# Performance work log

Hardware: AMD Instinct MI355X
Metric: run time of the kernel (lower is better)

## Reference

```python
import jax, jax.numpy as jnp
import numpy as np

B, H, W, C = 32, 56, 56, 256
K = 7  # spatial-attention conv kernel size


def setup_inputs() -> dict:
    key = jax.random.key(0)
    kx, kw = jax.random.split(key)
    x = jax.random.normal(kx, (B, H, W, C), dtype=jnp.float32)
    # he_normal init for a 7x7 conv with 2 input channels
    fan_in = K * K * 2
    conv_w = jax.random.normal(kw, (K, K, 2, 1), dtype=jnp.float32) * jnp.sqrt(2.0 / fan_in)
    return {"x": x, "conv_w": conv_w}


def reference(x, conv_w):
    # channel-wise avg and max pooling -> [B,H,W,2]
    avg_pool = jnp.mean(x, axis=-1, keepdims=True)
    max_pool = jnp.max(x, axis=-1, keepdims=True)
    concat = jnp.concatenate([avg_pool, max_pool], axis=-1)
    # 7x7 conv, 2 -> 1 channels, SAME padding, no bias, sigmoid activation
    attn = jax.lax.conv_general_dilated(
        concat, conv_w,
        window_strides=(1, 1), padding="SAME",
        dimension_numbers=("NHWC", "HWIO", "NHWC"),
    )
    attn = jax.nn.sigmoid(attn)  # [B,H,W,1]
    return x * attn
```

## Files before the change

### kernel.cpp

```cpp
#include <hip/hip_runtime.h>
#include <math.h>

#define BB 32
#define HH 56
#define WW 56
#define CC 256
#define KS 7
#define NPIX (BB * HH * WW)

__global__ __launch_bounds__(256) void pool_kernel(const float* __restrict__ x,
                                                   float2* __restrict__ pooled) {
    const int wave = threadIdx.x >> 6;
    const int lane = threadIdx.x & 63;
    const int pix = blockIdx.x * 4 + wave;
    if (pix >= NPIX) return;

    const float4 v = reinterpret_cast<const float4*>(x)[(size_t)pix * (CC / 4) + lane];
    float s = v.x + v.y + v.z + v.w;
    float m = fmaxf(fmaxf(v.x, v.y), fmaxf(v.z, v.w));

#pragma unroll
    for (int off = 32; off > 0; off >>= 1) {
        s += __shfl_down(s, off, 64);
        m = fmaxf(m, __shfl_down(m, off, 64));
    }
    if (lane == 0) {
        pooled[pix] = make_float2(s * (1.0f / CC), m);
    }
}

__global__ __launch_bounds__(256) void conv_kernel(const float2* __restrict__ pooled,
                                                   const float* __restrict__ cw,
                                                   float* __restrict__ attn) {
    const int pix = blockIdx.x * blockDim.x + threadIdx.x;
    if (pix >= NPIX) return;
    const int wcol = pix % WW;
    const int t = pix / WW;
    const int hrow = t % HH;
    const int b = t / HH;

    float acc = 0.0f;
#pragma unroll
    for (int ky = 0; ky < KS; ++ky) {
        const int yy = hrow + ky - 3;
        if (yy < 0 || yy >= HH) continue;
#pragma unroll
        for (int kx = 0; kx < KS; ++kx) {
            const int xx = wcol + kx - 3;
            if (xx < 0 || xx >= WW) continue;
            const float2 p = pooled[((size_t)b * HH + yy) * WW + xx];
            acc = fmaf(p.x, cw[(ky * KS + kx) * 2 + 0], acc);
            acc = fmaf(p.y, cw[(ky * KS + kx) * 2 + 1], acc);
        }
    }
    attn[pix] = 1.0f / (1.0f + expf(-acc));
}

__global__ __launch_bounds__(256) void mul_kernel(const float* __restrict__ x,
                                                  const float* __restrict__ attn,
                                                  float* __restrict__ out) {
    const size_t i = (size_t)blockIdx.x * blockDim.x + threadIdx.x;
    const float4 v = reinterpret_cast<const float4*>(x)[i];
    const float a = attn[i >> 6];
    float4 o;
    o.x = v.x * a;
    o.y = v.y * a;
    o.z = v.z * a;
    o.w = v.w * a;
    reinterpret_cast<float4*>(out)[i] = o;
}

extern "C" void kernel_launch(void* const* d_in, const int* in_sizes, int n_in,
                              void* d_out, int out_size, void* d_ws, size_t ws_size,
                              hipStream_t stream) {
    const float* x = (const float*)d_in[0];
    const float* cw = (const float*)d_in[1];
    float* out = (float*)d_out;

    float2* pooled = (float2*)d_ws;
    float* attn = (float*)((char*)d_ws + (size_t)NPIX * sizeof(float2));

    pool_kernel<<<NPIX / 4, 256, 0, stream>>>(x, pooled);

    conv_kernel<<<(NPIX + 255) / 256, 256, 0, stream>>>(pooled, cw, attn);

    const size_t n4 = (size_t)BB * HH * WW * CC / 4;
    mul_kernel<<<(unsigned)(n4 / 256), 256, 0, stream>>>(x, attn, out);
}
```

Before: 62.74 us.

## Fuse spatial conv and sigmoid into the broadcast-multiply kernel with wave-per-pixel taps

Replaces the separate conv and multiply kernels with one kernel where each wave handles a pixel: 49 lanes compute the 7x7 taps from the pooled map, reduce them with a cross-lane shuffle, apply the sigmoid, then scale the 256 channels. This removes one kernel launch and the intermediate attention buffer round trip. Output is written with nontemporal stores to reduce cache pollution. Each wave now repeats the conv reduction, adding ALU and shuffle work to a bandwidth-bound pass.

```diff
diff --git a/kernel.cpp b/kernel.cpp
--- a/kernel.cpp
+++ b/kernel.cpp
@@ -8,6 +8,8 @@
 #define KS 7
 #define NPIX (BB * HH * WW)
 
+typedef float vfloat4 __attribute__((ext_vector_type(4)));
+
 __global__ __launch_bounds__(256) void pool_kernel(const float* __restrict__ x,
                                                    float2* __restrict__ pooled) {
     const int wave = threadIdx.x >> 6;
@@ -15,7 +17,7 @@
     const int pix = blockIdx.x * 4 + wave;
     if (pix >= NPIX) return;
 
-    const float4 v = reinterpret_cast<const float4*>(x)[(size_t)pix * (CC / 4) + lane];
+    const vfloat4 v = reinterpret_cast<const vfloat4*>(x)[(size_t)pix * (CC / 4) + lane];
     float s = v.x + v.y + v.z + v.w;
     float m = fmaxf(fmaxf(v.x, v.y), fmaxf(v.z, v.w));
 
@@ -29,45 +31,41 @@
     }
 }
 
-__global__ __launch_bounds__(256) void conv_kernel(const float2* __restrict__ pooled,
-                                                   const float* __restrict__ cw,
-                                                   float* __restrict__ attn) {
-    const int pix = blockIdx.x * blockDim.x + threadIdx.x;
-    if (pix >= NPIX) return;
+__global__ __launch_bounds__(256) void fused_kernel(const float* __restrict__ x,
+                                                    const float2* __restrict__ pooled,
+                                                    const float2* __restrict__ cwv,
+                                                    float* __restrict__ out) {
+    const int wave = threadIdx.x >> 6;
+    const int lane = threadIdx.x & 63;
+    const int pix = blockIdx.x * 4 + wave;
+
     const int wcol = pix % WW;
     const int t = pix / WW;
     const int hrow = t % HH;
     const int b = t / HH;
 
-    float acc = 0.0f;
-#pragma unroll
-    for (int ky = 0; ky < KS; ++ky) {
+    float partial = 0.0f;
+    if (lane < KS * KS) {
+        const int ky = lane / KS;
+        const int kx = lane - ky * KS;
         const int yy = hrow + ky - 3;
-        if (yy < 0 || yy >= HH) continue;
-#pragma unroll
-        for (int kx = 0; kx < KS; ++kx) {
-            const int xx = wcol + kx - 3;
-            if (xx < 0 || xx >= WW) continue;
+        const int xx = wcol + kx - 3;
+        if (yy >= 0 && yy < HH && xx >= 0 && xx < WW) {
             const float2 p = pooled[((size_t)b * HH + yy) * WW + xx];
-            acc = fmaf(p.x, cw[(ky * KS + kx) * 2 + 0], acc);
-            acc = fmaf(p.y, cw[(ky * KS + kx) * 2 + 1], acc);
+            const float2 w = cwv[lane];
+            partial = fmaf(p.x, w.x, p.y * w.y);
         }
     }
-    attn[pix] = 1.0f / (1.0f + expf(-acc));
-}
+#pragma unroll
+    for (int off = 1; off < 64; off <<= 1) {
+        partial += __shfl_xor(partial, off, 64);
+    }
+    const float att = 1.0f / (1.0f + expf(-partial));
 
-__global__ __launch_bounds__(256) void mul_kernel(const float* __restrict__ x,
-                                                  const float* __restrict__ attn,
-                                                  float* __restrict__ out) {
-    const size_t i = (size_t)blockIdx.x * blockDim.x + threadIdx.x;
-    const float4 v = reinterpret_cast<const float4*>(x)[i];
-    const float a = attn[i >> 6];
-    float4 o;
-    o.x = v.x * a;
-    o.y = v.y * a;
-    o.z = v.z * a;
-    o.w = v.w * a;
-    reinterpret_cast<float4*>(out)[i] = o;
+    const size_t i = (size_t)pix * (CC / 4) + lane;
+    const vfloat4 v = reinterpret_cast<const vfloat4*>(x)[i];
+    vfloat4 o = v * att;
+    __builtin_nontemporal_store(o, reinterpret_cast<vfloat4*>(out) + i);
 }
 
 extern "C" void kernel_launch(void* const* d_in, const int* in_sizes, int n_in,
@@ -78,12 +76,8 @@
     float* out = (float*)d_out;
 
     float2* pooled = (float2*)d_ws;
-    float* attn = (float*)((char*)d_ws + (size_t)NPIX * sizeof(float2));
 
     pool_kernel<<<NPIX / 4, 256, 0, stream>>>(x, pooled);
 
-    conv_kernel<<<(NPIX + 255) / 256, 256, 0, stream>>>(pooled, cw, attn);
-
-    const size_t n4 = (size_t)BB * HH * WW * CC / 4;
-    mul_kernel<<<(unsigned)(n4 / 256), 256, 0, stream>>>(x, attn, out);
+    fused_kernel<<<NPIX / 4, 256, 0, stream>>>(x, pooled, (const float2*)cw, out);
 }
```

Result: faster. 54.87 us (-12.5%).
